# Performance work log

Hardware: AMD Instinct MI355X
Metric: run time of the kernel (lower is better)

Reference implementation:

```python
import jax, jax.numpy as jnp
import numpy as np

QMIN, QMAX = 0.0, 255.0  # uint8 activation quantization range


def _qlinear(x, w_q, b, s_in, zp_in, s_w):
    """zentorch_qlinear: quantize fp32 x to uint8, int8 weight, dequant output.

    x:   [M, K] fp32
    w_q: [N, K] int8 values (stored int32), symmetric (weight zp = 0)
    b:   [N] fp32
    s_in, zp_in: scalars (activation scale / zero point)
    s_w: [N] per-output-channel weight scales
    """
    zp = zp_in.astype(jnp.float32)
    q = jnp.clip(jnp.round(x / s_in) + zp, QMIN, QMAX)      # fake-quant uint8
    x_dq = (q - zp) * s_in                                   # dequantized activation
    w_dq = w_q.astype(jnp.float32) * s_w[:, None]            # [N, K] dequant weight
    return x_dq @ w_dq.T + b                                 # [M, N] fp32


def setup_inputs() -> dict:
    key = jax.random.key(0)
    k1, k2, k3, k4 = jax.random.split(key, 4)
    M, K, N = 8192, 4096, 4096
    inp = {
        "input": jax.random.normal(k1, (M, K), dtype=jnp.float32),
        "weights": jax.random.randint(k2, (N, K), -128, 128, dtype=jnp.int32),
        "biases": jax.random.normal(k3, (N,), dtype=jnp.float32) * 0.1,
        "input_scales": jnp.array([0.05], dtype=jnp.float32),
        "input_zero_points": jnp.array([128], dtype=jnp.int32),
        "weight_scales": jax.random.uniform(k4, (N,), dtype=jnp.float32, minval=0.001, maxval=0.01),
        "weight_zero_points": jnp.zeros((N,), dtype=jnp.int32),
        "output_dtype": 0,  # 0 -> float32
    }
    return inp


def reference(input, weights, biases, input_scales, input_zero_points,
              weight_scales, weight_zero_points, output_dtype):
    s_in = input_scales[0]
    zp_in = input_zero_points[0]
    x = _qlinear(input, weights, biases, s_in, zp_in, weight_scales)
    x = _qlinear(x, weights, biases, s_in, zp_in, weight_scales)
    x = _qlinear(x, weights, biases, s_in, zp_in, weight_scales)
    return x
```

## Files before the change

kernel.cpp:

```cpp
#include <hip/hip_runtime.h>
#include <stdint.h>

#define M_DIM 8192
#define K_DIM 4096
#define N_DIM 4096
#define KTILES (K_DIM / 64)

typedef __attribute__((ext_vector_type(4))) int i32x4;

__global__ void pack_w_kernel(const int* __restrict__ w, char* __restrict__ wp,
                              int* __restrict__ corr, const int* __restrict__ zpp) {
  __shared__ int red[256];
  const int n = blockIdx.x;
  const int t = threadIdx.x;
  const int4* row = (const int4*)(w + (size_t)n * K_DIM);
  int s = 0;
  int words[4];
#pragma unroll
  for (int u = 0; u < 4; ++u) {
    int4 v = row[t * 4 + u];
    s += v.x + v.y + v.z + v.w;
    words[u] = (v.x & 255) | ((v.y & 255) << 8) | ((v.z & 255) << 16) | (v.w << 24);
  }
  ((int4*)(wp + (size_t)n * K_DIM))[t] = make_int4(words[0], words[1], words[2], words[3]);
  red[t] = s;
  __syncthreads();
  for (int off = 128; off > 0; off >>= 1) {
    if (t < off) red[t] += red[t + off];
    __syncthreads();
  }
  if (t == 0) corr[n] = (128 - zpp[0]) * red[0];
}

__global__ void quant_in_kernel(const float* __restrict__ x, char* __restrict__ q,
                                const float* __restrict__ sp, const int* __restrict__ zpp) {
  const int i = blockIdx.x * blockDim.x + threadIdx.x;
  const float s = sp[0];
  const float zp = (float)zpp[0];
  float4 v = ((const float4*)x)[i];
  float t0 = fminf(fmaxf(rintf(v.x / s) + zp, 0.f), 255.f);
  float t1 = fminf(fmaxf(rintf(v.y / s) + zp, 0.f), 255.f);
  float t2 = fminf(fmaxf(rintf(v.z / s) + zp, 0.f), 255.f);
  float t3 = fminf(fmaxf(rintf(v.w / s) + zp, 0.f), 255.f);
  int b0 = (int)t0 - 128, b1 = (int)t1 - 128, b2 = (int)t2 - 128, b3 = (int)t3 - 128;
  ((int*)q)[i] = (b0 & 255) | ((b1 & 255) << 8) | ((b2 & 255) << 16) | (b3 << 24);
}

#define STAGE16(SRC, DST)                                                     \
  __builtin_amdgcn_global_load_lds(                                           \
      (const __attribute__((address_space(1))) void*)(SRC),                   \
      (__attribute__((address_space(3))) void*)(DST), 16, 0, 0)

#define RD(p) (*(const i32x4*)(p))

#define TILE2(SLOT, KN, DO_NEXT)                                              \
  {                                                                           \
    const char* cA_ = &lds[SLOT][0][0];                                       \
    char* nA_ = &lds[(SLOT) ^ 1][0][0];                                       \
    char* nB_ = &lds[(SLOT) ^ 1][1][0];                                       \
    i32x4 a1_[4];                                                             \
    _Pragma("unroll") for (int i_ = 0; i_ < 4; ++i_)                          \
        a1_[i_] = RD(cA_ + aoff[4 + i_]);                                     \
    if (DO_NEXT) {                                                            \
      STAGE16(asrc0 + (size_t)(KN), nA_ + o0_);                               \
      STAGE16(asrc1 + (size_t)(KN), nA_ + o1_);                               \
      STAGE16(bsrc0 + (size_t)(KN), nB_ + o0_);                               \
      STAGE16(bsrc1 + (size_t)(KN), nB_ + o1_);                               \
    }                                                                         \
    __builtin_amdgcn_s_setprio(1);                                            \
    _Pragma("unroll") for (int i_ = 0; i_ < 4; ++i_)                          \
        _Pragma("unroll") for (int j_ = 0; j_ < 4; ++j_)                      \
            acc[i_][j_] = __builtin_amdgcn_mfma_i32_16x16x64_i8(              \
                a0[i_], b0[j_], acc[i_][j_], 0, 0, 0);                        \
    __builtin_amdgcn_s_setprio(0);                                            \
    __builtin_amdgcn_s_setprio(1);                                            \
    _Pragma("unroll") for (int i_ = 0; i_ < 4; ++i_)                          \
        _Pragma("unroll") for (int j_ = 0; j_ < 4; ++j_)                      \
            acc[4 + i_][j_] = __builtin_amdgcn_mfma_i32_16x16x64_i8(          \
                a1_[i_], b0[j_], acc[4 + i_][j_], 0, 0, 0);                   \
    __builtin_amdgcn_s_setprio(0);                                            \
    asm volatile("s_waitcnt vmcnt(0)" ::: "memory");                          \
    __builtin_amdgcn_s_barrier();                                             \
    if (DO_NEXT) {                                                            \
      _Pragma("unroll") for (int i_ = 0; i_ < 4; ++i_)                        \
          a0[i_] = RD(nA_ + aoff[i_]);                                        \
      _Pragma("unroll") for (int j_ = 0; j_ < 4; ++j_)                        \
          b0[j_] = RD(nB_ + boff[j_]);                                        \
    }                                                                         \
  }

template <int WRITE_Q>
__global__ __launch_bounds__(512, 2) void gemm_kernel(
    const char* __restrict__ qa, const char* __restrict__ wb,
    const int* __restrict__ corr, const float* __restrict__ swp,
    const float* __restrict__ bias, const float* __restrict__ sp,
    const int* __restrict__ zpp, char* __restrict__ outq, float* __restrict__ outf) {
  __shared__ __align__(16) char lds[2][2][16384];
  const int tid = threadIdx.x;
  const int lane = tid & 63;
  const int w = tid >> 6;
  const int wr = w >> 2;
  const int wc = w & 3;
  const int bid = blockIdx.x;
  const int bm = bid & 31;
  const int bn = bid >> 5;
  const char* abase = qa + (size_t)bm * 256 * K_DIM;
  const char* bbase = wb + (size_t)bn * 256 * K_DIM;

  const int o0_ = tid * 16;
  const int o1_ = 8192 + tid * 16;
  const int r0_ = o0_ >> 6, r1_ = o1_ >> 6;
  const int g0_ = ((o0_ >> 4) & 3) ^ ((r0_ >> 1) & 3);
  const int g1_ = ((o1_ >> 4) & 3) ^ ((r1_ >> 1) & 3);
  const char* asrc0 = abase + (size_t)r0_ * K_DIM + g0_ * 16;
  const char* asrc1 = abase + (size_t)r1_ * K_DIM + g1_ * 16;
  const int p0_ = (r0_ & ~63) + 4 * (r0_ & 15) + ((r0_ >> 4) & 3);
  const int p1_ = (r1_ & ~63) + 4 * (r1_ & 15) + ((r1_ >> 4) & 3);
  const char* bsrc0 = bbase + (size_t)p0_ * K_DIM + g0_ * 16;
  const char* bsrc1 = bbase + (size_t)p1_ * K_DIM + g1_ * 16;

  const int rr = lane & 15;
  const int g = lane >> 4;
  int aoff[8], boff[4];
#pragma unroll
  for (int i = 0; i < 8; ++i) {
    const int row = wr * 128 + i * 16 + rr;
    aoff[i] = (row << 6) + ((g ^ ((row >> 1) & 3)) << 4);
  }
#pragma unroll
  for (int j = 0; j < 4; ++j) {
    const int row = wc * 64 + j * 16 + rr;
    boff[j] = (row << 6) + ((g ^ ((row >> 1) & 3)) << 4);
  }

  i32x4 acc[8][4] = {};

  STAGE16(asrc0, &lds[0][0][o0_]); STAGE16(asrc1, &lds[0][0][o1_]);
  STAGE16(bsrc0, &lds[0][1][o0_]); STAGE16(bsrc1, &lds[0][1][o1_]);
  asm volatile("s_waitcnt vmcnt(0)" ::: "memory");
  __builtin_amdgcn_s_barrier();

  i32x4 a0[4], b0[4];
#pragma unroll
  for (int i = 0; i < 4; ++i) a0[i] = RD(&lds[0][0][0] + aoff[i]);
#pragma unroll
  for (int j = 0; j < 4; ++j) b0[j] = RD(&lds[0][1][0] + boff[j]);

  for (int tb = 0; tb < (KTILES - 2) / 2; ++tb) {
    const size_t k0 = (size_t)(tb * 2 + 1) * 64;
    TILE2(0, k0, 1)
    TILE2(1, k0 + 64, 1)
  }
  TILE2(0, (size_t)(KTILES - 1) * 64, 1)
  TILE2(1, 0, 0)

  const float s = sp[0];
  const float zpf = (float)zpp[0];
  const int m0 = bm * 256 + wr * 128 + (lane >> 4) * 4;
  const int nb4 = bn * 256 + wc * 64 + ((lane & 15) << 2);
  const int4 cr4 = *(const int4*)(corr + nb4);
  const float4 sw4 = *(const float4*)(swp + nb4);
  const float4 bb4 = *(const float4*)(bias + nb4);
  const float fs0 = s * sw4.x, fs1 = s * sw4.y, fs2 = s * sw4.z, fs3 = s * sw4.w;
#pragma unroll
  for (int i = 0; i < 8; ++i) {
#pragma unroll
    for (int q = 0; q < 4; ++q) {
      const int m = m0 + i * 16 + q;
      const float v0 = fs0 * (float)(acc[i][0][q] + cr4.x) + bb4.x;
      const float v1 = fs1 * (float)(acc[i][1][q] + cr4.y) + bb4.y;
      const float v2 = fs2 * (float)(acc[i][2][q] + cr4.z) + bb4.z;
      const float v3 = fs3 * (float)(acc[i][3][q] + cr4.w) + bb4.w;
      if (WRITE_Q) {
        const int b0i = (int)fminf(fmaxf(rintf(v0 / s) + zpf, 0.f), 255.f) - 128;
        const int b1i = (int)fminf(fmaxf(rintf(v1 / s) + zpf, 0.f), 255.f) - 128;
        const int b2i = (int)fminf(fmaxf(rintf(v2 / s) + zpf, 0.f), 255.f) - 128;
        const int b3i = (int)fminf(fmaxf(rintf(v3 / s) + zpf, 0.f), 255.f) - 128;
        const uint32_t pk = (uint32_t)(b0i & 255) | ((uint32_t)(b1i & 255) << 8) |
                            ((uint32_t)(b2i & 255) << 16) | ((uint32_t)b3i << 24);
        *(uint32_t*)(outq + (size_t)m * N_DIM + nb4) = pk;
      } else {
        float4 o4;
        o4.x = v0; o4.y = v1; o4.z = v2; o4.w = v3;
        *(float4*)(outf + (size_t)m * N_DIM + nb4) = o4;
      }
    }
  }
}

extern "C" void kernel_launch(void* const* d_in, const int* in_sizes, int n_in,
                              void* d_out, int out_size, void* d_ws, size_t ws_size,
                              hipStream_t stream) {
  const float* x = (const float*)d_in[0];
  const int* wq = (const int*)d_in[1];
  const float* bias = (const float*)d_in[2];
  const float* s_in = (const float*)d_in[3];
  const int* zp_in = (const int*)d_in[4];
  const float* s_w = (const float*)d_in[5];
  float* out = (float*)d_out;

  const size_t WP_BYTES = (size_t)N_DIM * K_DIM;
  const size_t Q_BYTES = (size_t)M_DIM * K_DIM;
  char* ws = (char*)d_ws;
  char* wp = ws;
  char* q1 = ws + WP_BYTES;
  char* q2 = q1 + Q_BYTES;
  int* corr = (int*)(q2 + Q_BYTES);
  const size_t NEEDED = WP_BYTES + 2 * Q_BYTES + (size_t)N_DIM * sizeof(int);
  if (ws_size < NEEDED) return;

  pack_w_kernel<<<N_DIM, 256, 0, stream>>>(wq, wp, corr, zp_in);
  quant_in_kernel<<<(M_DIM * K_DIM / 4) / 256, 256, 0, stream>>>(x, q1, s_in, zp_in);

  dim3 grid((M_DIM / 256) * (N_DIM / 256));
  dim3 blk(512);
  gemm_kernel<1><<<grid, blk, 0, stream>>>(q1, wp, corr, s_w, bias, s_in, zp_in, q2, nullptr);
  gemm_kernel<1><<<grid, blk, 0, stream>>>(q2, wp, corr, s_w, bias, s_in, zp_in, q1, nullptr);
  gemm_kernel<0><<<grid, blk, 0, stream>>>(q1, wp, corr, s_w, bias, s_in, zp_in, nullptr, out);
}
```

Baseline: 453.1 us.

## Use 4-stage LDS ring with 1024-thread blocks and 64x64 per-wave tiles

Replaces the double-buffered LDS pipeline with a four-slot ring that prefetches three K tiles ahead. Block size doubles to 16 waves, and each wave now computes a 64x64 sub-tile instead of 128x64. Fragment loads now go straight from LDS into the MFMAs, with no register-level prefetch. The aim is to hide global-load latency better, at the cost of 128KB LDS per block, lower per-wave operand reuse and more barrier participants. The __launch_bounds__(1024,4) hint also risks forcing a tight register budget that could cause spills.

```diff
diff --git a/kernel.cpp b/kernel.cpp
--- a/kernel.cpp
+++ b/kernel.cpp
@@ -53,49 +53,36 @@
 
 #define RD(p) (*(const i32x4*)(p))
 
-#define TILE2(SLOT, KN, DO_NEXT)                                              \
+#define TILE4(SLOT, KS)                                                       \
   {                                                                           \
     const char* cA_ = &lds[SLOT][0][0];                                       \
-    char* nA_ = &lds[(SLOT) ^ 1][0][0];                                       \
-    char* nB_ = &lds[(SLOT) ^ 1][1][0];                                       \
-    i32x4 a1_[4];                                                             \
+    const char* cB_ = &lds[SLOT][1][0];                                       \
+    char* nA_ = &lds[((SLOT) + 3) & 3][0][0];                                 \
+    char* nB_ = &lds[((SLOT) + 3) & 3][1][0];                                 \
+    i32x4 a_[4], b_[4];                                                       \
     _Pragma("unroll") for (int i_ = 0; i_ < 4; ++i_)                          \
-        a1_[i_] = RD(cA_ + aoff[4 + i_]);                                     \
-    if (DO_NEXT) {                                                            \
-      STAGE16(asrc0 + (size_t)(KN), nA_ + o0_);                               \
-      STAGE16(asrc1 + (size_t)(KN), nA_ + o1_);                               \
-      STAGE16(bsrc0 + (size_t)(KN), nB_ + o0_);                               \
-      STAGE16(bsrc1 + (size_t)(KN), nB_ + o1_);                               \
-    }                                                                         \
+        a_[i_] = RD(cA_ + aoff[i_]);                                          \
+    _Pragma("unroll") for (int j_ = 0; j_ < 4; ++j_)                          \
+        b_[j_] = RD(cB_ + boff[j_]);                                          \
+    STAGE16(asrc0 + (size_t)(KS), nA_ + o0_);                                 \
+    STAGE16(bsrc0 + (size_t)(KS), nB_ + o0_);                                 \
     __builtin_amdgcn_s_setprio(1);                                            \
     _Pragma("unroll") for (int i_ = 0; i_ < 4; ++i_)                          \
         _Pragma("unroll") for (int j_ = 0; j_ < 4; ++j_)                      \
             acc[i_][j_] = __builtin_amdgcn_mfma_i32_16x16x64_i8(              \
-                a0[i_], b0[j_], acc[i_][j_], 0, 0, 0);                        \
+                a_[i_], b_[j_], acc[i_][j_], 0, 0, 0);                        \
     __builtin_amdgcn_s_setprio(0);                                            \
-    __builtin_amdgcn_s_setprio(1);                                            \
-    _Pragma("unroll") for (int i_ = 0; i_ < 4; ++i_)                          \
-        _Pragma("unroll") for (int j_ = 0; j_ < 4; ++j_)                      \
-            acc[4 + i_][j_] = __builtin_amdgcn_mfma_i32_16x16x64_i8(          \
-                a1_[i_], b0[j_], acc[4 + i_][j_], 0, 0, 0);                   \
-    __builtin_amdgcn_s_setprio(0);                                            \
-    asm volatile("s_waitcnt vmcnt(0)" ::: "memory");                          \
+    asm volatile("s_waitcnt vmcnt(2)" ::: "memory");                          \
     __builtin_amdgcn_s_barrier();                                             \
-    if (DO_NEXT) {                                                            \
-      _Pragma("unroll") for (int i_ = 0; i_ < 4; ++i_)                        \
-          a0[i_] = RD(nA_ + aoff[i_]);                                        \
-      _Pragma("unroll") for (int j_ = 0; j_ < 4; ++j_)                        \
-          b0[j_] = RD(nB_ + boff[j_]);                                        \
-    }                                                                         \
   }
 
 template <int WRITE_Q>
-__global__ __launch_bounds__(512, 2) void gemm_kernel(
+__global__ __launch_bounds__(1024, 4) void gemm_kernel(
     const char* __restrict__ qa, const char* __restrict__ wb,
     const int* __restrict__ corr, const float* __restrict__ swp,
     const float* __restrict__ bias, const float* __restrict__ sp,
     const int* __restrict__ zpp, char* __restrict__ outq, float* __restrict__ outf) {
-  __shared__ __align__(16) char lds[2][2][16384];
+  __shared__ __align__(16) char lds[4][2][16384];
   const int tid = threadIdx.x;
   const int lane = tid & 63;
   const int w = tid >> 6;
@@ -108,62 +95,53 @@
   const char* bbase = wb + (size_t)bn * 256 * K_DIM;
 
   const int o0_ = tid * 16;
-  const int o1_ = 8192 + tid * 16;
-  const int r0_ = o0_ >> 6, r1_ = o1_ >> 6;
-  const int g0_ = ((o0_ >> 4) & 3) ^ ((r0_ >> 1) & 3);
-  const int g1_ = ((o1_ >> 4) & 3) ^ ((r1_ >> 1) & 3);
+  const int r0_ = tid >> 2;
+  const int sl_ = tid & 3;
+  const int g0_ = sl_ ^ ((r0_ >> 1) & 3);
   const char* asrc0 = abase + (size_t)r0_ * K_DIM + g0_ * 16;
-  const char* asrc1 = abase + (size_t)r1_ * K_DIM + g1_ * 16;
   const int p0_ = (r0_ & ~63) + 4 * (r0_ & 15) + ((r0_ >> 4) & 3);
-  const int p1_ = (r1_ & ~63) + 4 * (r1_ & 15) + ((r1_ >> 4) & 3);
   const char* bsrc0 = bbase + (size_t)p0_ * K_DIM + g0_ * 16;
-  const char* bsrc1 = bbase + (size_t)p1_ * K_DIM + g1_ * 16;
 
   const int rr = lane & 15;
   const int g = lane >> 4;
-  int aoff[8], boff[4];
+  int aoff[4], boff[4];
 #pragma unroll
-  for (int i = 0; i < 8; ++i) {
-    const int row = wr * 128 + i * 16 + rr;
-    aoff[i] = (row << 6) + ((g ^ ((row >> 1) & 3)) << 4);
-  }
-#pragma unroll
-  for (int j = 0; j < 4; ++j) {
-    const int row = wc * 64 + j * 16 + rr;
-    boff[j] = (row << 6) + ((g ^ ((row >> 1) & 3)) << 4);
+  for (int i = 0; i < 4; ++i) {
+    const int rowA = wr * 64 + i * 16 + rr;
+    aoff[i] = (rowA << 6) + ((g ^ ((rowA >> 1) & 3)) << 4);
+    const int rowB = wc * 64 + i * 16 + rr;
+    boff[i] = (rowB << 6) + ((g ^ ((rowB >> 1) & 3)) << 4);
   }
 
-  i32x4 acc[8][4] = {};
+  i32x4 acc[4][4] = {};
 
-  STAGE16(asrc0, &lds[0][0][o0_]); STAGE16(asrc1, &lds[0][0][o1_]);
-  STAGE16(bsrc0, &lds[0][1][o0_]); STAGE16(bsrc1, &lds[0][1][o1_]);
-  asm volatile("s_waitcnt vmcnt(0)" ::: "memory");
+  STAGE16(asrc0, &lds[0][0][o0_]);       STAGE16(bsrc0, &lds[0][1][o0_]);
+  STAGE16(asrc0 + 64, &lds[1][0][o0_]);  STAGE16(bsrc0 + 64, &lds[1][1][o0_]);
+  STAGE16(asrc0 + 128, &lds[2][0][o0_]); STAGE16(bsrc0 + 128, &lds[2][1][o0_]);
+  asm volatile("s_waitcnt vmcnt(2)" ::: "memory");
   __builtin_amdgcn_s_barrier();
 
-  i32x4 a0[4], b0[4];
-#pragma unroll
-  for (int i = 0; i < 4; ++i) a0[i] = RD(&lds[0][0][0] + aoff[i]);
-#pragma unroll
-  for (int j = 0; j < 4; ++j) b0[j] = RD(&lds[0][1][0] + boff[j]);
-
-  for (int tb = 0; tb < (KTILES - 2) / 2; ++tb) {
-    const size_t k0 = (size_t)(tb * 2 + 1) * 64;
-    TILE2(0, k0, 1)
-    TILE2(1, k0 + 64, 1)
+#define KCL(x) ((size_t)((x) < KTILES ? (x) : KTILES - 1) * 64)
+  for (int tb = 0; tb < KTILES / 4; ++tb) {
+    const int t0 = tb * 4;
+    TILE4(0, KCL(t0 + 3))
+    TILE4(1, KCL(t0 + 4))
+    TILE4(2, KCL(t0 + 5))
+    TILE4(3, KCL(t0 + 6))
   }
-  TILE2(0, (size_t)(KTILES - 1) * 64, 1)
-  TILE2(1, 0, 0)
+#undef KCL
+  asm volatile("s_waitcnt vmcnt(0)" ::: "memory");
 
   const float s = sp[0];
   const float zpf = (float)zpp[0];
-  const int m0 = bm * 256 + wr * 128 + (lane >> 4) * 4;
+  const int m0 = bm * 256 + wr * 64 + (lane >> 4) * 4;
   const int nb4 = bn * 256 + wc * 64 + ((lane & 15) << 2);
   const int4 cr4 = *(const int4*)(corr + nb4);
   const float4 sw4 = *(const float4*)(swp + nb4);
   const float4 bb4 = *(const float4*)(bias + nb4);
   const float fs0 = s * sw4.x, fs1 = s * sw4.y, fs2 = s * sw4.z, fs3 = s * sw4.w;
 #pragma unroll
-  for (int i = 0; i < 8; ++i) {
+  for (int i = 0; i < 4; ++i) {
 #pragma unroll
     for (int q = 0; q < 4; ++q) {
       const int m = m0 + i * 16 + q;
@@ -213,7 +191,7 @@
   quant_in_kernel<<<(M_DIM * K_DIM / 4) / 256, 256, 0, stream>>>(x, q1, s_in, zp_in);
 
   dim3 grid((M_DIM / 256) * (N_DIM / 256));
-  dim3 blk(512);
+  dim3 blk(1024);
   gemm_kernel<1><<<grid, blk, 0, stream>>>(q1, wp, corr, s_w, bias, s_in, zp_in, q2, nullptr);
   gemm_kernel<1><<<grid, blk, 0, stream>>>(q2, wp, corr, s_w, bias, s_in, zp_in, q1, nullptr);
   gemm_kernel<0><<<grid, blk, 0, stream>>>(q1, wp, corr, s_w, bias, s_in, zp_in, nullptr, out);
```

Result: faster. 438.0 us, median of 2 (-3.3%).
